# Kernel optimization log

Measured on AMD Instinct MI355X. Metric: run time of the kernel, lower is better.

The kernel has to match this reference:

```python
import jax, jax.numpy as jnp
import numpy as np

B, S, D, H, DFF = 4, 1024, 1024, 16, 4096
DK = D // H
EPS = 1e-9


def _layernorm(x, alpha, bias):
    # Faithful to source: torch.std is unbiased (ddof=1), eps added to std.
    mean = jnp.mean(x, axis=-1, keepdims=True)
    xc = x - mean
    std = jnp.sqrt(jnp.sum(xc * xc, axis=-1, keepdims=True) / (x.shape[-1] - 1))
    return alpha * xc / (std + EPS) + bias


def _mha(x, wq_w, wq_b, wo_w, wo_b):
    # Source bug preserved: w_q is used for q, k, AND v projections.
    p = (x @ wq_w + wq_b).reshape(B, S, H, DK).transpose(0, 2, 1, 3)  # [B,H,S,DK]
    scores = jnp.einsum('bhqd,bhkd->bhqk', p, p) / jnp.sqrt(jnp.asarray(DK, x.dtype))
    attn = jax.nn.softmax(scores, axis=-1)
    out = jnp.einsum('bhqk,bhkd->bhqd', attn, p)
    out = out.transpose(0, 2, 1, 3).reshape(B, S, D)
    return out @ wo_w + wo_b


def _ffn(x, w1, b1, w2, b2):
    return jax.nn.relu(x @ w1 + b1) @ w2 + b2


def setup_inputs() -> dict:
    key = jax.random.key(0)
    ks = jax.random.split(key, 8)
    sc = 0.02
    return {
        'x': jax.random.normal(ks[0], (B, S, D), jnp.float32),
        'wq_w': sc * jax.random.normal(ks[1], (D, D), jnp.float32),
        'wq_b': jnp.zeros((D,), jnp.float32),
        'wo_w': sc * jax.random.normal(ks[2], (D, D), jnp.float32),
        'wo_b': jnp.zeros((D,), jnp.float32),
        'ff1_w': sc * jax.random.normal(ks[3], (D, DFF), jnp.float32),
        'ff1_b': jnp.zeros((DFF,), jnp.float32),
        'ff2_w': sc * jax.random.normal(ks[4], (DFF, D), jnp.float32),
        'ff2_b': jnp.zeros((D,), jnp.float32),
        'alpha1': jnp.ones((1,), jnp.float32), 'bias1': jnp.zeros((1,), jnp.float32),
        'alpha2': jnp.ones((1,), jnp.float32), 'bias2': jnp.zeros((1,), jnp.float32),
        'alpha3': jnp.ones((1,), jnp.float32), 'bias3': jnp.zeros((1,), jnp.float32),
    }


def reference(x, wq_w, wq_b, wo_w, wo_b, ff1_w, ff1_b, ff2_w, ff2_b,
              alpha1, bias1, alpha2, bias2, alpha3, bias3):
    h1 = x + _mha(_layernorm(x, alpha1, bias1), wq_w, wq_b, wo_w, wo_b)
    h2 = h1 + _ffn(_layernorm(h1, alpha2, bias2), ff1_w, ff1_b, ff2_w, ff2_b)
    return _layernorm(h2, alpha3, bias3)
```

## Files before the change

### kernel.cpp

```cpp
#include <hip/hip_runtime.h>

typedef short short8 __attribute__((ext_vector_type(8)));
typedef float f32x4 __attribute__((ext_vector_type(4)));
typedef unsigned short u16x4 __attribute__((ext_vector_type(4)));

#define DEV static __device__ __forceinline__

DEV float b2f(unsigned short u) { return __uint_as_float(((unsigned)u) << 16); }
DEV unsigned short f2b(float f) {
    unsigned u = __float_as_uint(f);
    u += 0x7FFFu + ((u >> 16) & 1u);
    return (unsigned short)(u >> 16);
}
DEV float wred_sum(float v) {
#pragma unroll
    for (int o = 32; o; o >>= 1) v += __shfl_xor(v, o);
    return v;
}

DEV void gld_lds16(const unsigned short* g, unsigned short* l) {
    __builtin_amdgcn_global_load_lds((const __attribute__((address_space(1))) void*)g,
                                     (__attribute__((address_space(3))) void*)l, 16, 0, 0);
}

template <bool IN_BF16, bool OUT_BF16>
__global__ __launch_bounds__(256) void ln_kernel(const void* __restrict__ in_v,
                                                 void* __restrict__ out_v,
                                                 const float* __restrict__ alpha_p,
                                                 const float* __restrict__ bias_p) {
    __shared__ float redA[4], redB[4];
    const int row = blockIdx.x;
    const int t = threadIdx.x;
    const int lane = t & 63, w = t >> 6;

    float x0, x1, x2, x3;
    if (IN_BF16) {
        u16x4 raw = *(const u16x4*)&((const unsigned short*)in_v)[(size_t)row * 1024 + t * 4];
        x0 = b2f(raw[0]); x1 = b2f(raw[1]); x2 = b2f(raw[2]); x3 = b2f(raw[3]);
    } else {
        f32x4 xv = *(const f32x4*)&((const float*)in_v)[(size_t)row * 1024 + t * 4];
        x0 = xv[0]; x1 = xv[1]; x2 = xv[2]; x3 = xv[3];
    }

    float s = wred_sum(x0 + x1 + x2 + x3);
    if (lane == 0) redA[w] = s;
    __syncthreads();
    float mean = (redA[0] + redA[1] + redA[2] + redA[3]) * (1.0f / 1024.0f);

    float d0 = x0 - mean, d1 = x1 - mean, d2 = x2 - mean, d3 = x3 - mean;
    float ss = wred_sum(d0 * d0 + d1 * d1 + d2 * d2 + d3 * d3);
    if (lane == 0) redB[w] = ss;
    __syncthreads();
    float var = (redB[0] + redB[1] + redB[2] + redB[3]) * (1.0f / 1023.0f);
    float denom = sqrtf(var) + 1e-9f;
    float inv = alpha_p[0] / denom;
    float bias = bias_p[0];

    if (OUT_BF16) {
        u16x4 o;
        o[0] = f2b(d0 * inv + bias);
        o[1] = f2b(d1 * inv + bias);
        o[2] = f2b(d2 * inv + bias);
        o[3] = f2b(d3 * inv + bias);
        *(u16x4*)&((unsigned short*)out_v)[(size_t)row * 1024 + t * 4] = o;
    } else {
        f32x4 o;
        o[0] = d0 * inv + bias;
        o[1] = d1 * inv + bias;
        o[2] = d2 * inv + bias;
        o[3] = d3 * inv + bias;
        *(f32x4*)&((float*)out_v)[(size_t)row * 1024 + t * 4] = o;
    }
}

__global__ __launch_bounds__(256) void prelude_kernel(
    const float* __restrict__ x, unsigned short* __restrict__ lnbuf,
    const float* __restrict__ alpha1, const float* __restrict__ bias1,
    const float* __restrict__ wq_w, unsigned short* __restrict__ wq_t,
    const float* __restrict__ wo_w, unsigned short* __restrict__ wo_t,
    const float* __restrict__ ff1_w, unsigned short* __restrict__ ff1_t,
    const float* __restrict__ ff2_w, unsigned short* __restrict__ ff2_t) {
    __shared__ unsigned short tile[32][33];
    __shared__ float redA[4], redB[4];
    const int t = threadIdx.x;
    int bid = blockIdx.x;

    if (bid < 4096) {
        const int row = bid;
        const int lane = t & 63, w = t >> 6;
        f32x4 xv = *(const f32x4*)&x[(size_t)row * 1024 + t * 4];
        float s = wred_sum(xv[0] + xv[1] + xv[2] + xv[3]);
        if (lane == 0) redA[w] = s;
        __syncthreads();
        float mean = (redA[0] + redA[1] + redA[2] + redA[3]) * (1.0f / 1024.0f);
        float d0 = xv[0] - mean, d1 = xv[1] - mean, d2 = xv[2] - mean, d3 = xv[3] - mean;
        float ss = wred_sum(d0 * d0 + d1 * d1 + d2 * d2 + d3 * d3);
        if (lane == 0) redB[w] = ss;
        __syncthreads();
        float var = (redB[0] + redB[1] + redB[2] + redB[3]) * (1.0f / 1023.0f);
        float inv = alpha1[0] / (sqrtf(var) + 1e-9f);
        float bias = bias1[0];
        u16x4 o;
        o[0] = f2b(d0 * inv + bias);
        o[1] = f2b(d1 * inv + bias);
        o[2] = f2b(d2 * inv + bias);
        o[3] = f2b(d3 * inv + bias);
        *(u16x4*)&lnbuf[(size_t)row * 1024 + t * 4] = o;
        return;
    }
    bid -= 4096;
    const float* src;
    unsigned short* dst;
    int R, C, gx;
    if (bid < 1024) {
        src = wq_w; dst = wq_t; R = 1024; C = 1024; gx = 32;
    } else if (bid < 2048) {
        bid -= 1024; src = wo_w; dst = wo_t; R = 1024; C = 1024; gx = 32;
    } else if (bid < 6144) {
        bid -= 2048; src = ff1_w; dst = ff1_t; R = 1024; C = 4096; gx = 128;
    } else {
        bid -= 6144; src = ff2_w; dst = ff2_t; R = 4096; C = 1024; gx = 32;
    }
    const int c0 = (bid % gx) * 32, r0 = (bid / gx) * 32;
    const int xx = t & 31, y0 = t >> 5;
#pragma unroll
    for (int yy = y0; yy < 32; yy += 8) tile[yy][xx] = f2b(src[(size_t)(r0 + yy) * C + c0 + xx]);
    __syncthreads();
#pragma unroll
    for (int yy = y0; yy < 32; yy += 8) dst[(size_t)(c0 + yy) * R + r0 + xx] = tile[xx][yy];
}

template <int BM, int BN, bool RELU, int RES_MODE, bool OUT_BF16, bool WRITE_T>
__global__ __launch_bounds__(512, 4) void gemm2d(const unsigned short* __restrict__ A,
                                                 const unsigned short* __restrict__ Bt,
                                                 const float* __restrict__ bias,
                                                 const void* __restrict__ res,
                                                 void* __restrict__ C_v,
                                                 unsigned short* __restrict__ Ct,
                                                 int M, int N, int K) {
    constexpr int WM = BM / 4, WN = BN / 2;
    constexpr int FM = WM / 16, FN = WN / 16;
    __shared__ __align__(16) unsigned short As[3][BM * 64];
    __shared__ __align__(16) unsigned short Bs[3][BN * 64];

    const int t = threadIdx.x;
    const int lane = t & 63, wid = t >> 6;
    const int wr = wid >> 1, wc = wid & 1;
    const int lr = lane & 15, g = lane >> 4;

    const int nwg = gridDim.x;
    const int cpx = nwg >> 3;
    const int wg = blockIdx.x;
    const int swz = (wg & 7) * cpx + (wg >> 3);
    const int NB = N / BN;
    const int m0 = (swz / NB) * BM, n0 = (swz % NB) * BN;

    f32x4 acc[FM][FN];
#pragma unroll
    for (int i = 0; i < FM; ++i)
#pragma unroll
        for (int j = 0; j < FN; ++j) acc[i][j] = (f32x4)0.0f;

    const int NT = K / 64;

#define STAGE2D(kt)                                                                        \
    {                                                                                      \
        const int buf_ = (kt) % 3;                                                         \
        const int k0_ = (kt) * 64;                                                         \
        _Pragma("unroll") for (int s = 0; s < BM / 64; ++s) {                              \
            int id = s * 512 + t;                                                          \
            int row = id >> 3, ch = (id & 7) ^ (row & 7);                                  \
            gld_lds16(&A[(size_t)(m0 + row) * K + k0_ + ch * 8],                           \
                      &As[buf_][(size_t)(s * 512 + (t & ~63)) * 8]);                       \
        }                                                                                  \
        {                                                                                  \
            int row = t >> 3, ch = (t & 7) ^ (row & 7);                                    \
            gld_lds16(&Bt[(size_t)(n0 + row) * K + k0_ + ch * 8],                          \
                      &Bs[buf_][(size_t)(t & ~63) * 8]);                                   \
        }                                                                                  \
    }

    STAGE2D(0);
    STAGE2D(1);
    asm volatile("s_waitcnt vmcnt(3)" ::: "memory");
    __builtin_amdgcn_sched_barrier(0);
    __builtin_amdgcn_s_barrier();

    for (int kt = 0; kt < NT; ++kt) {
        const int buf = kt % 3;
        if (kt + 2 < NT) STAGE2D(kt + 2);

        short8 af[FM][2], bfr[FN][2];
#pragma unroll
        for (int mi = 0; mi < FM; ++mi) {
            int row = wr * WM + mi * 16 + lr;
#pragma unroll
            for (int ks = 0; ks < 2; ++ks) {
                int ch = (ks * 4 + g) ^ (row & 7);
                af[mi][ks] = *(const short8*)&As[buf][row * 64 + ch * 8];
            }
        }
#pragma unroll
        for (int ni = 0; ni < FN; ++ni) {
            int row = wc * WN + ni * 16 + lr;
#pragma unroll
            for (int ks = 0; ks < 2; ++ks) {
                int ch = (ks * 4 + g) ^ (row & 7);
                bfr[ni][ks] = *(const short8*)&Bs[buf][row * 64 + ch * 8];
            }
        }

        __builtin_amdgcn_s_setprio(1);
#pragma unroll
        for (int ks = 0; ks < 2; ++ks)
#pragma unroll
            for (int mi = 0; mi < FM; ++mi)
#pragma unroll
                for (int ni = 0; ni < FN; ++ni)
                    acc[mi][ni] = __builtin_amdgcn_mfma_f32_16x16x32_bf16(af[mi][ks], bfr[ni][ks], acc[mi][ni], 0, 0, 0);
        __builtin_amdgcn_s_setprio(0);

        if (kt + 2 < NT) {
            asm volatile("s_waitcnt vmcnt(3)" ::: "memory");
        } else if (kt + 1 < NT) {
            asm volatile("s_waitcnt vmcnt(0)" ::: "memory");
        }
        __builtin_amdgcn_sched_barrier(0);
        __builtin_amdgcn_s_barrier();
    }
#undef STAGE2D

    const int lg = g;
#pragma unroll
    for (int ni = 0; ni < FN; ++ni) {
        int col = n0 + wc * WN + ni * 16 + lr;
        float bv = bias[col];
#pragma unroll
        for (int mi = 0; mi < FM; ++mi) {
            int row0 = m0 + wr * WM + mi * 16 + lg * 4;
            u16x4 tv;
#pragma unroll
            for (int i = 0; i < 4; ++i) {
                int row = row0 + i;
                float x = acc[mi][ni][i] + bv;
                if (RES_MODE == 1) x += ((const float*)res)[(size_t)row * N + col];
                if (RES_MODE == 2) x += b2f(((const unsigned short*)res)[(size_t)row * N + col]);
                if (RELU) x = fmaxf(x, 0.0f);
                if (OUT_BF16) {
                    unsigned short v = f2b(x);
                    ((unsigned short*)C_v)[(size_t)row * N + col] = v;
                    if (WRITE_T) tv[i] = v;
                } else {
                    ((float*)C_v)[(size_t)row * N + col] = x;
                }
            }
            if (WRITE_T) {
                int bb = row0 >> 10, s = row0 & 1023;
                *(u16x4*)&Ct[(size_t)bb * (1024 * 1024) + (size_t)col * 1024 + s] = tv;
            }
        }
    }
}

template <bool RELU, bool OUT_BF16>
__global__ __launch_bounds__(512, 4) void gemm3b(const unsigned short* __restrict__ A,
                                                 const unsigned short* __restrict__ Bt,
                                                 const float* __restrict__ bias,
                                                 void* __restrict__ C_v,
                                                 int M, int N, int K) {
    __shared__ __align__(16) unsigned short As[3][256 * 32];
    __shared__ __align__(16) unsigned short Bs[3][128 * 32];

    const int t = threadIdx.x;
    const int lane = t & 63;
    const int wid = t >> 6;
    const int wr = wid >> 1, wc = wid & 1;
    const int lr = lane & 15, g = lane >> 4;

    const int nwg = gridDim.x;
    const int cpx = nwg >> 3;
    const int wg = blockIdx.x;
    const int swz = (wg & 7) * cpx + (wg >> 3);
    const int NB = N / 128;
    const int m0 = (swz / NB) * 256, n0 = (swz % NB) * 128;

    f32x4 acc[4][4];
#pragma unroll
    for (int i = 0; i < 4; ++i)
#pragma unroll
        for (int j = 0; j < 4; ++j) acc[i][j] = (f32x4)0.0f;

    const int NT = K / 32;

#define STAGE3B(kt)                                                                         \
    {                                                                                       \
        const int buf_ = (kt) % 3;                                                          \
        const int k0_ = (kt) * 32;                                                          \
        _Pragma("unroll") for (int s = 0; s < 2; ++s) {                                     \
            int id = s * 512 + t;                                                           \
            int row = id >> 2;                                                              \
            int ch = (id & 3) ^ ((row >> 1) & 3);                                           \
            gld_lds16(&A[(size_t)(m0 + row) * K + k0_ + ch * 8],                            \
                      &As[buf_][(size_t)(s * 512 + (t & ~63)) * 8]);                        \
        }                                                                                   \
        {                                                                                   \
            int row = t >> 2;                                                               \
            int ch = (t & 3) ^ ((row >> 1) & 3);                                            \
            gld_lds16(&Bt[(size_t)(n0 + row) * K + k0_ + ch * 8],                           \
                      &Bs[buf_][(size_t)(t & ~63) * 8]);                                    \
        }                                                                                   \
    }

    STAGE3B(0);
    STAGE3B(1);
    asm volatile("s_waitcnt vmcnt(3)" ::: "memory");
    __builtin_amdgcn_sched_barrier(0);
    __builtin_amdgcn_s_barrier();

    for (int kt = 0; kt < NT; ++kt) {
        const int buf = kt % 3;
        if (kt + 2 < NT) STAGE3B(kt + 2);

        short8 af[4], bf[4];
#pragma unroll
        for (int mi = 0; mi < 4; ++mi) {
            int row = wr * 64 + mi * 16 + lr;
            int ch = g ^ ((row >> 1) & 3);
            af[mi] = *(const short8*)&As[buf][row * 32 + ch * 8];
        }
#pragma unroll
        for (int nj = 0; nj < 4; ++nj) {
            int row = wc * 64 + nj * 16 + lr;
            int ch = g ^ ((row >> 1) & 3);
            bf[nj] = *(const short8*)&Bs[buf][row * 32 + ch * 8];
        }

        __builtin_amdgcn_s_setprio(1);
#pragma unroll
        for (int mi = 0; mi < 4; ++mi)
#pragma unroll
            for (int nj = 0; nj < 4; ++nj)
                acc[mi][nj] = __builtin_amdgcn_mfma_f32_16x16x32_bf16(af[mi], bf[nj], acc[mi][nj], 0, 0, 0);
        __builtin_amdgcn_s_setprio(0);

        if (kt + 2 < NT) {
            asm volatile("s_waitcnt vmcnt(3)" ::: "memory");
        } else if (kt + 1 < NT) {
            asm volatile("s_waitcnt vmcnt(0)" ::: "memory");
        }
        __builtin_amdgcn_sched_barrier(0);
        __builtin_amdgcn_s_barrier();
    }
#undef STAGE3B

#pragma unroll
    for (int nj = 0; nj < 4; ++nj) {
        int col = n0 + wc * 64 + nj * 16 + lr;
        float bv = bias[col];
#pragma unroll
        for (int mi = 0; mi < 4; ++mi) {
            int row0 = m0 + wr * 64 + mi * 16 + g * 4;
#pragma unroll
            for (int i = 0; i < 4; ++i) {
                int row = row0 + i;
                float x = acc[mi][nj][i] + bv;
                if (RELU) x = fmaxf(x, 0.0f);
                if (OUT_BF16)
                    ((unsigned short*)C_v)[(size_t)row * N + col] = f2b(x);
                else
                    ((float*)C_v)[(size_t)row * N + col] = x;
            }
        }
    }
}

__global__ __launch_bounds__(512) void attn_mfma_kernel(const unsigned short* __restrict__ p,
                                                        const unsigned short* __restrict__ pT,
                                                        unsigned short* __restrict__ out) {
    __shared__ __align__(16) unsigned short Ks[128 * 64];
    __shared__ __align__(16) unsigned short Vt[64 * 128];
    __shared__ __align__(16) unsigned short Ps[8 * 16 * 64];

    const int t = threadIdx.x;
    const int lane = t & 63, w = t >> 6;
    const int lr = lane & 15, g = lane >> 4;
    const int bh = blockIdx.x;
    const int qblk = blockIdx.y;
    const int b = bh >> 4, h = bh & 15;

    const unsigned short* Pm = p + (size_t)b * (1024 * 1024) + h * 64;
    const unsigned short* PT = pT + (size_t)b * (1024 * 1024) + (size_t)(h * 64) * 1024;

    const int q0 = qblk * 128 + w * 16;
    short8 qa0 = *(const short8*)&Pm[(size_t)(q0 + lr) * 1024 + g * 8];
    short8 qa1 = *(const short8*)&Pm[(size_t)(q0 + lr) * 1024 + 32 + g * 8];

    f32x4 acc[4];
#pragma unroll
    for (int i = 0; i < 4; ++i) acc[i] = (f32x4)0.0f;
    float mrow[4] = {-1e30f, -1e30f, -1e30f, -1e30f};
    float lsum[4] = {0.f, 0.f, 0.f, 0.f};

    unsigned short* Pw = &Ps[w * 16 * 64];
    const float C2 = 0.18033688011112042f;

    for (int kt = 0; kt < 8; ++kt) {
        const int key0 = kt * 128;
        __syncthreads();
#pragma unroll
        for (int i = 0; i < 2; ++i) {
            int id = i * 512 + t;
            int row = id >> 3, ch = (id & 7) * 8;
            int sw = ch ^ ((row & 7) << 3);
            short8 kv = *(const short8*)&Pm[(size_t)(key0 + row) * 1024 + ch];
            *(short8*)&Ks[row * 64 + sw] = kv;
        }
#pragma unroll
        for (int i = 0; i < 2; ++i) {
            int id = i * 512 + t;
            int row = id >> 4, ch = id & 15;
            int sw = (ch ^ (row & 7)) * 8;
            short8 vv = *(const short8*)&PT[(size_t)row * 1024 + key0 + ch * 8];
            *(short8*)&Vt[row * 128 + sw] = vv;
        }
        __syncthreads();

        f32x4 s_acc[8];
        __builtin_amdgcn_s_setprio(1);
#pragma unroll
        for (int kg = 0; kg < 8; ++kg) {
            s_acc[kg] = (f32x4)0.0f;
            int krow = kg * 16 + lr;
            int swz = (krow & 7) << 3;
            short8 kb0 = *(const short8*)&Ks[krow * 64 + ((g * 8) ^ swz)];
            short8 kb1 = *(const short8*)&Ks[krow * 64 + ((32 + g * 8) ^ swz)];
            s_acc[kg] = __builtin_amdgcn_mfma_f32_16x16x32_bf16(qa0, kb0, s_acc[kg], 0, 0, 0);
            s_acc[kg] = __builtin_amdgcn_mfma_f32_16x16x32_bf16(qa1, kb1, s_acc[kg], 0, 0, 0);
        }
        __builtin_amdgcn_s_setprio(0);

#pragma unroll
        for (int reg = 0; reg < 4; ++reg) {
            float mx = fmaxf(fmaxf(fmaxf(s_acc[0][reg], s_acc[1][reg]),
                                   fmaxf(s_acc[2][reg], s_acc[3][reg])),
                             fmaxf(fmaxf(s_acc[4][reg], s_acc[5][reg]),
                                   fmaxf(s_acc[6][reg], s_acc[7][reg])));
            mx = fmaxf(mx, __shfl_xor(mx, 1));
            mx = fmaxf(mx, __shfl_xor(mx, 2));
            mx = fmaxf(mx, __shfl_xor(mx, 4));
            mx = fmaxf(mx, __shfl_xor(mx, 8));
            float mnew = fmaxf(mrow[reg], mx * C2);
            float scale = __builtin_exp2f(mrow[reg] - mnew);
            mrow[reg] = mnew;
            float ps = 0.f;
#pragma unroll
            for (int kg = 0; kg < 8; ++kg) {
                float pv = __builtin_exp2f(fmaf(s_acc[kg][reg], C2, -mnew));
                s_acc[kg][reg] = pv;
                ps += pv;
            }
            lsum[reg] = lsum[reg] * scale + ps;
#pragma unroll
            for (int dg = 0; dg < 4; ++dg) acc[dg][reg] *= scale;
        }

#pragma unroll
        for (int hh = 0; hh < 2; ++hh) {
#pragma unroll
            for (int reg = 0; reg < 4; ++reg) {
                int q = g * 4 + reg;
                int swz = (q & 7) << 3;
#pragma unroll
                for (int kg = 0; kg < 4; ++kg) {
                    int key = lr + 16 * kg;
                    Pw[q * 64 + (key ^ swz)] = f2b(s_acc[hh * 4 + kg][reg]);
                }
            }
            int pswz = (lr & 7) << 3;
            short8 pa0 = *(const short8*)&Pw[lr * 64 + ((g * 8) ^ pswz)];
            short8 pa1 = *(const short8*)&Pw[lr * 64 + ((32 + g * 8) ^ pswz)];

            __builtin_amdgcn_s_setprio(1);
#pragma unroll
            for (int dg = 0; dg < 4; ++dg) {
                int drow = dg * 16 + lr;
                int c0 = (hh * 8 + g) ^ (drow & 7);
                int c1 = (hh * 8 + 4 + g) ^ (drow & 7);
                short8 vb0 = *(const short8*)&Vt[drow * 128 + c0 * 8];
                short8 vb1 = *(const short8*)&Vt[drow * 128 + c1 * 8];
                acc[dg] = __builtin_amdgcn_mfma_f32_16x16x32_bf16(pa0, vb0, acc[dg], 0, 0, 0);
                acc[dg] = __builtin_amdgcn_mfma_f32_16x16x32_bf16(pa1, vb1, acc[dg], 0, 0, 0);
            }
            __builtin_amdgcn_s_setprio(0);
        }
    }

    unsigned short* O = out + (size_t)b * (1024 * 1024) + h * 64;
#pragma unroll
    for (int reg = 0; reg < 4; ++reg) {
        float ls = lsum[reg];
        ls += __shfl_xor(ls, 1);
        ls += __shfl_xor(ls, 2);
        ls += __shfl_xor(ls, 4);
        ls += __shfl_xor(ls, 8);
        float inv = 1.0f / ls;
        int q = q0 + g * 4 + reg;
#pragma unroll
        for (int dg = 0; dg < 4; ++dg) {
            O[(size_t)q * 1024 + dg * 16 + lr] = f2b(acc[dg][reg] * inv);
        }
    }
}

extern "C" void kernel_launch(void* const* d_in, const int* in_sizes, int n_in,
                              void* d_out, int out_size, void* d_ws, size_t ws_size,
                              hipStream_t stream) {
    const float* x = (const float*)d_in[0];
    const float* wq_w = (const float*)d_in[1];
    const float* wq_b = (const float*)d_in[2];
    const float* wo_w = (const float*)d_in[3];
    const float* wo_b = (const float*)d_in[4];
    const float* ff1_w = (const float*)d_in[5];
    const float* ff1_b = (const float*)d_in[6];
    const float* ff2_w = (const float*)d_in[7];
    const float* ff2_b = (const float*)d_in[8];
    const float* alpha1 = (const float*)d_in[9];
    const float* bias1 = (const float*)d_in[10];
    const float* alpha2 = (const float*)d_in[11];
    const float* bias2 = (const float*)d_in[12];
    const float* alpha3 = (const float*)d_in[13];
    const float* bias3 = (const float*)d_in[14];
    float* out = (float*)d_out;

    const size_t MB = 1u << 20;
    char* ws = (char*)d_ws;
    unsigned short* wq_t = (unsigned short*)(ws + 0 * MB);
    unsigned short* wo_t = (unsigned short*)(ws + 2 * MB);
    unsigned short* ff1_t = (unsigned short*)(ws + 4 * MB);
    unsigned short* ff2_t = (unsigned short*)(ws + 12 * MB);
    unsigned short* lnbuf = (unsigned short*)(ws + 20 * MB);
    unsigned short* pbuf = (unsigned short*)(ws + 28 * MB);
    unsigned short* attn = (unsigned short*)(ws + 36 * MB);
    unsigned short* h1 = (unsigned short*)(ws + 44 * MB);
    unsigned short* h2 = (unsigned short*)(ws + 52 * MB);
    unsigned short* pbT = (unsigned short*)(ws + 60 * MB);
    unsigned short* mid = (unsigned short*)(ws + 60 * MB);

    const int M = 4096;

    prelude_kernel<<<14336, 256, 0, stream>>>(x, lnbuf, alpha1, bias1,
                                              wq_w, wq_t, wo_w, wo_t,
                                              ff1_w, ff1_t, ff2_w, ff2_t);
    gemm2d<128, 64, false, 0, true, true><<<512, 512, 0, stream>>>(lnbuf, wq_t, wq_b, nullptr, pbuf, pbT, M, 1024, 1024);
    attn_mfma_kernel<<<dim3(64, 8), 512, 0, stream>>>(pbuf, pbT, attn);
    gemm2d<128, 64, false, 1, true, false><<<512, 512, 0, stream>>>(attn, wo_t, wo_b, x, h1, nullptr, M, 1024, 1024);
    ln_kernel<true, true><<<M, 256, 0, stream>>>(h1, lnbuf, alpha2, bias2);
    gemm3b<true, true><<<512, 512, 0, stream>>>(lnbuf, ff1_t, ff1_b, mid, M, 4096, 1024);
    gemm2d<128, 64, false, 2, true, false><<<512, 512, 0, stream>>>(mid, ff2_t, ff2_b, h1, h2, nullptr, M, 1024, 4096);
    ln_kernel<true, false><<<M, 256, 0, stream>>>(h2, out, alpha3, bias3);
}
```

Baseline: 207.3 us.

## Load GEMM B operand directly to registers, bypassing LDS, double-buffered

Result: slower. 361.8 us (+74.5%).

```diff
diff --git a/kernel.cpp b/kernel.cpp
--- a/kernel.cpp
+++ b/kernel.cpp
@@ -131,7 +131,7 @@
 }
 
 template <int BM, int BN, bool RELU, int RES_MODE, bool OUT_BF16, bool WRITE_T>
-__global__ __launch_bounds__(512, 4) void gemm2d(const unsigned short* __restrict__ A,
+__global__ __launch_bounds__(512, 6) void gemm2e(const unsigned short* __restrict__ A,
                                                  const unsigned short* __restrict__ Bt,
                                                  const float* __restrict__ bias,
                                                  const void* __restrict__ res,
@@ -141,7 +141,6 @@
     constexpr int WM = BM / 4, WN = BN / 2;
     constexpr int FM = WM / 16, FN = WN / 16;
     __shared__ __align__(16) unsigned short As[3][BM * 64];
-    __shared__ __align__(16) unsigned short Bs[3][BN * 64];
 
     const int t = threadIdx.x;
     const int lane = t & 63, wid = t >> 6;
@@ -163,7 +162,10 @@
 
     const int NT = K / 64;
 
-#define STAGE2D(kt)                                                                        \
+    const unsigned short* brow0 = &Bt[(size_t)(n0 + wc * WN + 0 * 16 + lr) * K];
+    const unsigned short* brow1 = &Bt[(size_t)(n0 + wc * WN + 1 * 16 + lr) * K];
+
+#define STAGEA(kt)                                                                         \
     {                                                                                      \
         const int buf_ = (kt) % 3;                                                         \
         const int k0_ = (kt) * 64;                                                         \
@@ -173,62 +175,73 @@
             gld_lds16(&A[(size_t)(m0 + row) * K + k0_ + ch * 8],                           \
                       &As[buf_][(size_t)(s * 512 + (t & ~63)) * 8]);                       \
         }                                                                                  \
-        {                                                                                  \
-            int row = t >> 3, ch = (t & 7) ^ (row & 7);                                    \
-            gld_lds16(&Bt[(size_t)(n0 + row) * K + k0_ + ch * 8],                          \
-                      &Bs[buf_][(size_t)(t & ~63) * 8]);                                   \
+    }
+
+#define LOADB(dst, kt)                                                                     \
+    {                                                                                      \
+        const int k0_ = (kt) * 64;                                                         \
+        dst[0][0] = *(const short8*)&brow0[k0_ + g * 8];                                   \
+        dst[0][1] = *(const short8*)&brow0[k0_ + 32 + g * 8];                              \
+        dst[1][0] = *(const short8*)&brow1[k0_ + g * 8];                                   \
+        dst[1][1] = *(const short8*)&brow1[k0_ + 32 + g * 8];                              \
+    }
+
+#define COMPUTE(kt, bcur)                                                                  \
+    {                                                                                      \
+        const int buf_ = (kt) % 3;                                                         \
+        short8 af_[FM][2];                                                                 \
+        _Pragma("unroll") for (int mi = 0; mi < FM; ++mi) {                                \
+            int row = wr * WM + mi * 16 + lr;                                              \
+            _Pragma("unroll") for (int ks = 0; ks < 2; ++ks) {                             \
+                int ch = (ks * 4 + g) ^ (row & 7);                                         \
+                af_[mi][ks] = *(const short8*)&As[buf_][row * 64 + ch * 8];                \
+            }                                                                              \
         }                                                                                  \
-    }
-
-    STAGE2D(0);
-    STAGE2D(1);
-    asm volatile("s_waitcnt vmcnt(3)" ::: "memory");
+        __builtin_amdgcn_s_setprio(1);                                                     \
+        _Pragma("unroll") for (int ks = 0; ks < 2; ++ks)                                   \
+            _Pragma("unroll") for (int mi = 0; mi < FM; ++mi)                              \
+                _Pragma("unroll") for (int ni = 0; ni < FN; ++ni)                          \
+                    acc[mi][ni] = __builtin_amdgcn_mfma_f32_16x16x32_bf16(                 \
+                        af_[mi][ks], bcur[ni][ks], acc[mi][ni], 0, 0, 0);                  \
+        __builtin_amdgcn_s_setprio(0);                                                     \
+    }
+
+    short8 bA[2][2], bB[2][2];
+
+    LOADB(bA, 0);
+    STAGEA(0);
+    STAGEA(1);
+    asm volatile("s_waitcnt vmcnt(2)" ::: "memory");
     __builtin_amdgcn_sched_barrier(0);
     __builtin_amdgcn_s_barrier();
 
-    for (int kt = 0; kt < NT; ++kt) {
-        const int buf = kt % 3;
-        if (kt + 2 < NT) STAGE2D(kt + 2);
-
-        short8 af[FM][2], bfr[FN][2];
-#pragma unroll
-        for (int mi = 0; mi < FM; ++mi) {
-            int row = wr * WM + mi * 16 + lr;
-#pragma unroll
-            for (int ks = 0; ks < 2; ++ks) {
-                int ch = (ks * 4 + g) ^ (row & 7);
-                af[mi][ks] = *(const short8*)&As[buf][row * 64 + ch * 8];
-            }
-        }
-#pragma unroll
-        for (int ni = 0; ni < FN; ++ni) {
-            int row = wc * WN + ni * 16 + lr;
-#pragma unroll
-            for (int ks = 0; ks < 2; ++ks) {
-                int ch = (ks * 4 + g) ^ (row & 7);
-                bfr[ni][ks] = *(const short8*)&Bs[buf][row * 64 + ch * 8];
-            }
-        }
-
-        __builtin_amdgcn_s_setprio(1);
-#pragma unroll
-        for (int ks = 0; ks < 2; ++ks)
-#pragma unroll
-            for (int mi = 0; mi < FM; ++mi)
-#pragma unroll
-                for (int ni = 0; ni < FN; ++ni)
-                    acc[mi][ni] = __builtin_amdgcn_mfma_f32_16x16x32_bf16(af[mi][ks], bfr[ni][ks], acc[mi][ni], 0, 0, 0);
-        __builtin_amdgcn_s_setprio(0);
-
-        if (kt + 2 < NT) {
-            asm volatile("s_waitcnt vmcnt(3)" ::: "memory");
-        } else if (kt + 1 < NT) {
-            asm volatile("s_waitcnt vmcnt(0)" ::: "memory");
-        }
+    for (int kt2 = 0; kt2 < NT / 2 - 1; ++kt2) {
+        const int kt = 2 * kt2;
+        STAGEA(kt + 2);
+        LOADB(bB, kt + 1);
+        COMPUTE(kt, bA);
+        asm volatile("s_waitcnt vmcnt(6)" ::: "memory");
         __builtin_amdgcn_sched_barrier(0);
         __builtin_amdgcn_s_barrier();
-    }
-#undef STAGE2D
+        STAGEA(kt + 3);
+        LOADB(bA, kt + 2);
+        COMPUTE(kt + 1, bB);
+        asm volatile("s_waitcnt vmcnt(6)" ::: "memory");
+        __builtin_amdgcn_sched_barrier(0);
+        __builtin_amdgcn_s_barrier();
+    }
+    {
+        const int kt = NT - 2;
+        LOADB(bB, kt + 1);
+        COMPUTE(kt, bA);
+        asm volatile("s_waitcnt vmcnt(0)" ::: "memory");
+        __builtin_amdgcn_sched_barrier(0);
+        __builtin_amdgcn_s_barrier();
+        COMPUTE(kt + 1, bB);
+    }
+#undef STAGEA
+#undef LOADB
+#undef COMPUTE
 
     const int lg = g;
 #pragma unroll
@@ -551,11 +564,11 @@
     prelude_kernel<<<14336, 256, 0, stream>>>(x, lnbuf, alpha1, bias1,
                                               wq_w, wq_t, wo_w, wo_t,
                                               ff1_w, ff1_t, ff2_w, ff2_t);
-    gemm2d<128, 64, false, 0, true, true><<<512, 512, 0, stream>>>(lnbuf, wq_t, wq_b, nullptr, pbuf, pbT, M, 1024, 1024);
+    gemm2e<128, 64, false, 0, true, true><<<512, 512, 0, stream>>>(lnbuf, wq_t, wq_b, nullptr, pbuf, pbT, M, 1024, 1024);
     attn_mfma_kernel<<<dim3(64, 8), 512, 0, stream>>>(pbuf, pbT, attn);
-    gemm2d<128, 64, false, 1, true, false><<<512, 512, 0, stream>>>(attn, wo_t, wo_b, x, h1, nullptr, M, 1024, 1024);
+    gemm2e<128, 64, false, 1, true, false><<<512, 512, 0, stream>>>(attn, wo_t, wo_b, x, h1, nullptr, M, 1024, 1024);
     ln_kernel<true, true><<<M, 256, 0, stream>>>(h1, lnbuf, alpha2, bias2);
     gemm3b<true, true><<<512, 512, 0, stream>>>(lnbuf, ff1_t, ff1_b, mid, M, 4096, 1024);
-    gemm2d<128, 64, false, 2, true, false><<<512, 512, 0, stream>>>(mid, ff2_t, ff2_b, h1, h2, nullptr, M, 1024, 4096);
+    gemm2e<128, 64, false, 2, true, false><<<512, 512, 0, stream>>>(mid, ff2_t, ff2_b, h1, h2, nullptr, M, 1024, 4096);
     ln_kernel<true, false><<<M, 256, 0, stream>>>(h2, out, alpha3, bias3);
 }
```
